# Kernel tuning notes

Measured on AMD Instinct MI355X. Metric: run time of the kernel, lower is better.

The kernel has to match this reference:

```python
import jax, jax.numpy as jnp
import numpy as np

D_MODEL = 1024
N_HEADS = 16
D_K = D_MODEL // N_HEADS
D_FF = 4096
EPS = 1e-5


def setup_inputs() -> dict:
    key = jax.random.key(0)
    ks = jax.random.split(key, 16)
    s = 0.02
    d, f = D_MODEL, D_FF
    return {
        'ebd_x': jax.random.normal(ks[0], (2, 2048, d), jnp.float32),
        'Wq': jax.random.normal(ks[1], (d, d), jnp.float32) * s,
        'bq': jnp.zeros((d,), jnp.float32),
        'Wk': jax.random.normal(ks[2], (d, d), jnp.float32) * s,
        'bk': jnp.zeros((d,), jnp.float32),
        'Wv': jax.random.normal(ks[3], (d, d), jnp.float32) * s,
        'bv': jnp.zeros((d,), jnp.float32),
        'Wo': jax.random.normal(ks[4], (d, d), jnp.float32) * s,
        'bo': jnp.zeros((d,), jnp.float32),
        'W1': jax.random.normal(ks[5], (d, f), jnp.float32) * s,
        'b1': jnp.zeros((f,), jnp.float32),
        'W2': jax.random.normal(ks[6], (f, d), jnp.float32) * s,
        'b2': jnp.zeros((d,), jnp.float32),
        'g1': jnp.ones((d,), jnp.float32),
        'beta1': jnp.zeros((d,), jnp.float32),
        'g2': jnp.ones((d,), jnp.float32),
        'beta2': jnp.zeros((d,), jnp.float32),
    }


def _layernorm(x, g, b):
    mu = jnp.mean(x, axis=-1, keepdims=True)
    var = jnp.mean(jnp.square(x - mu), axis=-1, keepdims=True)
    return (x - mu) * jax.lax.rsqrt(var + EPS) * g + b


def reference(ebd_x, Wq, bq, Wk, bk, Wv, bv, Wo, bo, W1, b1, W2, b2, g1, beta1, g2, beta2):
    b, L, d = ebd_x.shape
    h, dk = N_HEADS, D_K
    # QKV projections, split heads: (b, h, L, dk)
    q = (ebd_x @ Wq + bq).reshape(b, L, h, dk).transpose(0, 2, 1, 3)
    k = (ebd_x @ Wk + bk).reshape(b, L, h, dk).transpose(0, 2, 1, 3)
    v = (ebd_x @ Wv + bv).reshape(b, L, h, dk).transpose(0, 2, 1, 3)
    scores = jnp.einsum('bhLd,bhld->bhLl', q, k) / jnp.sqrt(jnp.float32(dk))
    attn = jax.nn.softmax(scores, axis=-1)
    attn_v = jnp.einsum('bhLl,bhld->bhLd', attn, v)
    # faithful to source: reshape (b,h,L,dk) -> (b,L,d) WITHOUT transposing back
    attn_v = attn_v.reshape(b, L, d)
    attn_v = attn_v @ Wo + bo
    # dropout is identity in eval mode
    x1 = _layernorm(attn_v + ebd_x, g1, beta1)
    ff = jax.nn.gelu(x1 @ W1 + b1, approximate=False) @ W2 + b2
    return _layernorm(ff + x1, g2, beta2)
```

## Files before the change

### kernel.cpp

```cpp
#include <hip/hip_runtime.h>
#include <hip/hip_bf16.h>
#include <math.h>

typedef __bf16 bhalf;
typedef __bf16 bhalf8 __attribute__((ext_vector_type(8)));
typedef float  floatx4 __attribute__((ext_vector_type(4)));
typedef float  floatx8 __attribute__((ext_vector_type(8)));
typedef unsigned short ushort_t;
typedef unsigned short ushort8 __attribute__((ext_vector_type(8)));

#define MFMA16(a, b, c) __builtin_amdgcn_mfma_f32_16x16x32_bf16((a), (b), (c), 0, 0, 0)

__device__ __forceinline__ void gload_lds16(const bhalf* g, bhalf* l)
{
    __builtin_amdgcn_global_load_lds((const __attribute__((address_space(1))) void*)g,
                                     (__attribute__((address_space(3))) void*)l, 16, 0, 0);
}

enum { EPI_PLAIN = 0, EPI_RES = 1, EPI_GELU = 2, EPI_QKV = 3 };

__global__ __launch_bounds__(256) void detect_dtype(const ushort_t* __restrict__ x,
                                                    int* __restrict__ flag)
{
    __shared__ int tot;
    if (threadIdx.x == 0) tot = 0;
    __syncthreads();
    int cnt = 0;
#pragma unroll
    for (int it = 0; it < 8; ++it) {
        const ushort8 u = *(const ushort8*)(x + ((size_t)(it * 256 + threadIdx.x)) * 8);
#pragma unroll
        for (int j = 0; j < 8; j += 2) {
            const int e = (u[j] >> 7) & 0xFF;
            if (e >= 0x90) ++cnt;
        }
    }
    atomicAdd(&tot, cnt);
    __syncthreads();
    if (threadIdx.x == 0) flag[0] = (tot > 64) ? 1 : 0;
}

__global__ __launch_bounds__(256) void norm_x(const void* __restrict__ s,
                                              bhalf* __restrict__ d,
                                              const int* __restrict__ flag)
{
    const int i = (blockIdx.x * 256 + threadIdx.x) * 8;
    if (*flag) {
        const floatx8 v = *(const floatx8*)((const float*)s + i);
        bhalf8 o;
#pragma unroll
        for (int j = 0; j < 8; ++j) o[j] = (bhalf)v[j];
        *(bhalf8*)(d + i) = o;
    } else {
        *(ushort8*)((ushort_t*)d + i) = *(const ushort8*)((const ushort_t*)s + i);
    }
}

struct Cvt { const void* s; bhalf* d; int n; };
struct CvtArr { Cvt t[10]; };

__global__ __launch_bounds__(256) void norm_vec(CvtArr a, const int* __restrict__ flag)
{
    const Cvt c = a.t[blockIdx.y];
    const int i = (blockIdx.x * 256 + threadIdx.x) * 8;
    if (i >= c.n) return;
    if (*flag) {
        const floatx8 v = *(const floatx8*)((const float*)c.s + i);
        bhalf8 o;
#pragma unroll
        for (int j = 0; j < 8; ++j) o[j] = (bhalf)v[j];
        *(bhalf8*)(c.d + i) = o;
    } else {
        *(ushort8*)((ushort_t*)c.d + i) = *(const ushort8*)((const ushort_t*)c.s + i);
    }
}

struct TDesc { const void* src; bhalf* dst; int R, C; };
struct TDescArr { TDesc t[6]; };

__global__ __launch_bounds__(256) void transpose_all(TDescArr a, const int* __restrict__ flag)
{
    __shared__ bhalf sm[32][33];
    const int id = blockIdx.x;
    TDesc d;
    int rem;
    if (id < 4096)      { d = a.t[id >> 10]; rem = id & 1023; }
    else if (id < 8192) { d = a.t[4];        rem = id - 4096; }
    else                { d = a.t[5];        rem = id - 8192; }
    const int txc = d.C >> 5;
    const int bx = (rem % txc) * 32;
    const int by = (rem / txc) * 32;
    const int tx = threadIdx.x & 31;
    const int ty = threadIdx.x >> 5;
    if (*flag) {
        const float* fin = (const float*)d.src;
#pragma unroll
        for (int i = 0; i < 4; ++i)
            sm[ty + i * 8][tx] = (bhalf)fin[(size_t)(by + ty + i * 8) * d.C + bx + tx];
    } else {
        const bhalf* bin = (const bhalf*)d.src;
#pragma unroll
        for (int i = 0; i < 4; ++i)
            sm[ty + i * 8][tx] = bin[(size_t)(by + ty + i * 8) * d.C + bx + tx];
    }
    __syncthreads();
#pragma unroll
    for (int i = 0; i < 4; ++i)
        d.dst[(size_t)(bx + ty + i * 8) * d.R + by + tx] = sm[tx][ty + i * 8];
}

__global__ __launch_bounds__(256) void vt_transpose(const bhalf* __restrict__ Vw,
                                                    bhalf* __restrict__ Vt)
{
    __shared__ bhalf sm[32][33];
    const int bh = blockIdx.z;
    const int b = bh >> 4, h = bh & 15;
    const int tb = blockIdx.y * 32;
    const int db = blockIdx.x * 32;
    const int tx = threadIdx.x & 31;
    const int ty = threadIdx.x >> 5;
#pragma unroll
    for (int i = 0; i < 4; ++i)
        sm[ty + i * 8][tx] = Vw[(size_t)(b * 2048 + tb + ty + i * 8) * 1024 + h * 64 + db + tx];
    __syncthreads();
#pragma unroll
    for (int i = 0; i < 4; ++i)
        Vt[(size_t)(bh * 64 + db + ty + i * 8) * 2048 + tb + tx] = sm[tx][ty + i * 8];
}

template <int EPI, int TN>
__global__ __launch_bounds__(256) void gemm128(
    const bhalf* __restrict__ A, int lda,
    const bhalf* __restrict__ BT, int ldb,
    const bhalf* __restrict__ bias,
    const bhalf* __restrict__ resid,
    bhalf* __restrict__ C, int ldc, int K,
    bhalf* __restrict__ Ck, bhalf* __restrict__ Cv)
{
    __shared__ __align__(16) bhalf As[128 * 64];
    __shared__ __align__(16) bhalf Bs[TN * 64];

    const int tid  = threadIdx.x;
    const int lane = tid & 63;
    const int w    = tid >> 6;
    const int l15  = lane & 15;
    const int q    = lane >> 4;
    constexpr int MT = (TN == 128) ? 4 : 2;
    const int wm   = (TN == 128) ? (w >> 1) * 64 : w * 32;
    const int wn   = (TN == 128) ? (w & 1) * 64 : 0;
    const int n0   = blockIdx.x * TN;
    const int m0   = blockIdx.y * 128;

    const int r8 = lane >> 3;
    const int c8 = lane & 7;
    const int gc = (c8 ^ r8) << 3;

    floatx4 acc[MT][4];
#pragma unroll
    for (int i = 0; i < MT; ++i)
#pragma unroll
        for (int j = 0; j < 4; ++j) acc[i][j] = (floatx4){0.f, 0.f, 0.f, 0.f};

    for (int k0 = 0; k0 < K; k0 += 64) {
        __syncthreads();
#pragma unroll
        for (int i = 0; i < 4; ++i) {
            const int rb = w * 32 + i * 8;
            gload_lds16(A + (size_t)(m0 + rb + r8) * lda + k0 + gc, &As[rb * 64] + lane * 8);
        }
        if constexpr (TN == 128) {
#pragma unroll
            for (int i = 0; i < 4; ++i) {
                const int rb = w * 32 + i * 8;
                gload_lds16(BT + (size_t)(n0 + rb + r8) * ldb + k0 + gc, &Bs[rb * 64] + lane * 8);
            }
        } else {
#pragma unroll
            for (int i = 0; i < 2; ++i) {
                const int rb = w * 16 + i * 8;
                gload_lds16(BT + (size_t)(n0 + rb + r8) * ldb + k0 + gc, &Bs[rb * 64] + lane * 8);
            }
        }
        __syncthreads();
#pragma unroll
        for (int s = 0; s < 2; ++s) {
            const int pc = (((s * 4 + q) ^ (l15 & 7)) << 3);
            bhalf8 af[MT], bf[4];
#pragma unroll
            for (int mt = 0; mt < MT; ++mt)
                af[mt] = *(const bhalf8*)&As[(wm + mt * 16 + l15) * 64 + pc];
#pragma unroll
            for (int nt = 0; nt < 4; ++nt)
                bf[nt] = *(const bhalf8*)&Bs[(wn + nt * 16 + l15) * 64 + pc];
#pragma unroll
            for (int mt = 0; mt < MT; ++mt)
#pragma unroll
                for (int nt = 0; nt < 4; ++nt)
                    acc[mt][nt] = MFMA16(af[mt], bf[nt], acc[mt][nt]);
        }
    }

#pragma unroll
    for (int mt = 0; mt < MT; ++mt)
#pragma unroll
        for (int nt = 0; nt < 4; ++nt) {
            const int col = n0 + wn + nt * 16 + l15;
            const float bv = (float)bias[col];
#pragma unroll
            for (int r = 0; r < 4; ++r) {
                const int row = m0 + wm + mt * 16 + q * 4 + r;
                float v = acc[mt][nt][r] + bv;
                if constexpr (EPI == EPI_PLAIN) {
                    C[(size_t)row * ldc + col] = (bhalf)v;
                } else if constexpr (EPI == EPI_RES) {
                    v += (float)resid[(size_t)row * ldc + col];
                    C[(size_t)row * ldc + col] = (bhalf)v;
                } else if constexpr (EPI == EPI_GELU) {
                    v = 0.5f * v * (1.f + erff(v * 0.70710678118654752f));
                    C[(size_t)row * ldc + col] = (bhalf)v;
                } else {
                    if (col < 1024)       C [(size_t)row * 1024 + col]        = (bhalf)v;
                    else if (col < 2048)  Ck[(size_t)row * 1024 + col - 1024] = (bhalf)v;
                    else                  Cv[(size_t)row * 1024 + col - 2048] = (bhalf)v;
                }
            }
        }
}

__global__ __launch_bounds__(256) void flash_attn(
    const bhalf* __restrict__ Q, const bhalf* __restrict__ Km,
    const bhalf* __restrict__ Vt, bhalf* __restrict__ ctx)
{
    __shared__ __align__(16) bhalf Ks[2][64 * 64];
    __shared__ __align__(16) bhalf Vs[2][64 * 64];
    __shared__ __align__(16) bhalf Ps[64 * 64];

    const int tid  = threadIdx.x;
    const int lane = tid & 63;
    const int wq   = tid >> 6;
    const int l15  = lane & 15;
    const int q    = lane >> 4;
    const int bh   = blockIdx.x & 31;
    const int l0   = (blockIdx.x >> 5) * 64;
    const int b    = bh >> 4, h = bh & 15;
    const float SC = 0.125f * 1.44269504f;

    const bhalf* qp = Q + ((size_t)(b * 2048 + l0 + wq * 16 + l15)) * 1024 + h * 64 + q * 8;
    const bhalf8 aQ0 = *(const bhalf8*)qp;
    const bhalf8 aQ1 = *(const bhalf8*)(qp + 32);

    float ps[4] = {0.f, 0.f, 0.f, 0.f};
    floatx4 o[4];
#pragma unroll
    for (int ot = 0; ot < 4; ++ot) o[ot] = (floatx4){0.f, 0.f, 0.f, 0.f};

    const int r8 = lane >> 3;
    const int c8 = lane & 7;
    const int gc = (c8 ^ r8) << 3;
    const bhalf* kbase = Km + ((size_t)(b * 2048)) * 1024 + h * 64;
    const bhalf* vbase = Vt + ((size_t)(bh * 64)) * 2048;

    auto stage = [&](int buf, int kt) {
#pragma unroll
        for (int i = 0; i < 2; ++i) {
            const int rb = wq * 16 + i * 8;
            gload_lds16(kbase + (size_t)(kt + rb + r8) * 1024 + gc, &Ks[buf][rb * 64] + lane * 8);
            gload_lds16(vbase + (size_t)(rb + r8) * 2048 + kt + gc, &Vs[buf][rb * 64] + lane * 8);
        }
    };

    stage(0, 0);
    int cur = 0;
    for (int kt = 0; kt < 2048; kt += 64) {
        __syncthreads();
        if (kt + 64 < 2048) stage(cur ^ 1, kt + 64);

        floatx4 s[4];
#pragma unroll
        for (int nt = 0; nt < 4; ++nt) {
            s[nt] = (floatx4){0.f, 0.f, 0.f, 0.f};
            bhalf8 bK0 = *(const bhalf8*)&Ks[cur][(nt * 16 + l15) * 64 + ((q ^ (l15 & 7)) << 3)];
            bhalf8 bK1 = *(const bhalf8*)&Ks[cur][(nt * 16 + l15) * 64 + (((4 + q) ^ (l15 & 7)) << 3)];
            s[nt] = MFMA16(aQ0, bK0, s[nt]);
            s[nt] = MFMA16(aQ1, bK1, s[nt]);
        }
#pragma unroll
        for (int nt = 0; nt < 4; ++nt)
#pragma unroll
            for (int r = 0; r < 4; ++r) {
                const float pv = __builtin_amdgcn_exp2f(fmaf(s[nt][r], SC, -8.f));
                ps[r] += pv;
                const int row = wq * 16 + q * 4 + r;
                const int pc = (2 * nt + (l15 >> 3)) ^ ((q * 4 + r) & 7);
                Ps[row * 64 + pc * 8 + (l15 & 7)] = (bhalf)pv;
            }

#pragma unroll
        for (int kc = 0; kc < 2; ++kc) {
            bhalf8 aP = *(const bhalf8*)&Ps[(wq * 16 + l15) * 64 + (((kc * 4 + q) ^ (l15 & 7)) << 3)];
#pragma unroll
            for (int ot = 0; ot < 4; ++ot) {
                bhalf8 bV = *(const bhalf8*)&Vs[cur][(ot * 16 + l15) * 64 + (((kc * 4 + q) ^ (l15 & 7)) << 3)];
                o[ot] = MFMA16(aP, bV, o[ot]);
            }
        }
        cur ^= 1;
    }

    float inv[4];
#pragma unroll
    for (int r = 0; r < 4; ++r) {
#pragma unroll
        for (int off = 1; off < 16; off <<= 1) ps[r] += __shfl_xor(ps[r], off);
        inv[r] = 1.f / ps[r];
    }
#pragma unroll
    for (int ot = 0; ot < 4; ++ot)
#pragma unroll
        for (int r = 0; r < 4; ++r) {
            const int l = l0 + wq * 16 + q * 4 + r;
            const int kk = ot * 16 + l15;
            const int R = h * 128 + (l >> 4);
            const int Cc = (l & 15) * 64 + kk;
            ctx[((size_t)(b * 2048 + R)) * 1024 + Cc] = (bhalf)(o[ot][r] * inv[r]);
        }
}

__global__ __launch_bounds__(256) void ln_kernel(
    const bhalf* __restrict__ X, const bhalf* __restrict__ g,
    const bhalf* __restrict__ be, void* __restrict__ out, const int* __restrict__ flag)
{
    __shared__ float red[4][2];
    const int tid = threadIdx.x;
    const int wid = tid >> 6;
    const int rid = tid >> 7;
    const int lt  = tid & 127;
    const int row = blockIdx.x * 2 + rid;
    const int col = lt * 8;
    const bhalf8 xv = *(const bhalf8*)(X + (size_t)row * 1024 + col);
    float v[8], s1 = 0.f, s2 = 0.f;
#pragma unroll
    for (int i = 0; i < 8; ++i) {
        v[i] = (float)xv[i];
        s1 += v[i];
        s2 += v[i] * v[i];
    }
#pragma unroll
    for (int off = 1; off < 64; off <<= 1) {
        s1 += __shfl_xor(s1, off);
        s2 += __shfl_xor(s2, off);
    }
    if ((tid & 63) == 0) { red[wid][0] = s1; red[wid][1] = s2; }
    __syncthreads();
    const float t1 = red[rid * 2][0] + red[rid * 2 + 1][0];
    const float t2 = red[rid * 2][1] + red[rid * 2 + 1][1];
    const float mu = t1 * (1.f / 1024.f);
    const float rs = rsqrtf(t2 * (1.f / 1024.f) - mu * mu + 1e-5f);
    const bool f32 = flag && (*flag != 0);
    if (f32) {
        floatx8 ov;
#pragma unroll
        for (int i = 0; i < 8; ++i)
            ov[i] = ((v[i] - mu) * rs) * (float)g[col + i] + (float)be[col + i];
        *(floatx8*)((float*)out + (size_t)row * 1024 + col) = ov;
    } else {
        bhalf8 ov;
#pragma unroll
        for (int i = 0; i < 8; ++i)
            ov[i] = (bhalf)(((v[i] - mu) * rs) * (float)g[col + i] + (float)be[col + i]);
        *(bhalf8*)((bhalf*)out + (size_t)row * 1024 + col) = ov;
    }
}

extern "C" void kernel_launch(void* const* d_in, const int* in_sizes, int n_in,
                              void* d_out, int out_size, void* d_ws, size_t ws_size,
                              hipStream_t stream)
{
    (void)in_sizes; (void)n_in; (void)out_size; (void)ws_size;

    char* p = (char*)d_ws;
    const size_t MB = 1024 * 1024;
    int*   flag  = (int*)p;
    bhalf* vecs  = (bhalf*)(p + 128 * 1024);
    bhalf* Qw    = (bhalf*)(p + 1 * MB);
    bhalf* Kw    = (bhalf*)(p + 9 * MB);
    bhalf* Vw    = (bhalf*)(p + 17 * MB);
    bhalf* Vt    = (bhalf*)(p + 25 * MB);
    bhalf* x_n   = (bhalf*)(p + 33 * MB);
    bhalf* WqkvT = (bhalf*)(p + 41 * MB);
    bhalf* WoT   = (bhalf*)(p + 47 * MB);
    bhalf* W1T   = (bhalf*)(p + 49 * MB);
    bhalf* W2T   = (bhalf*)(p + 57 * MB);
    bhalf* ctx   = Vw;
    bhalf* ff1   = (bhalf*)(p + 17 * MB);
    bhalf* ln1   = Qw;
    bhalf* x1    = Kw;
    bhalf* ff2   = Qw;

    bhalf* bqkv  = vecs;
    bhalf* bo_n  = vecs + 1 * 4096;
    bhalf* b1_n  = vecs + 2 * 4096;
    bhalf* b2_n  = vecs + 3 * 4096;
    bhalf* g1_n  = vecs + 4 * 4096;
    bhalf* be1_n = vecs + 5 * 4096;
    bhalf* g2_n  = vecs + 6 * 4096;
    bhalf* be2_n = vecs + 7 * 4096;

    const dim3 blk(256);

    detect_dtype<<<1, blk, 0, stream>>>((const ushort_t*)d_in[0], flag);

    norm_x<<<2048, blk, 0, stream>>>(d_in[0], x_n, flag);
    CvtArr arr;
    arr.t[0] = {d_in[2],  bqkv,        1024};
    arr.t[1] = {d_in[4],  bqkv + 1024, 1024};
    arr.t[2] = {d_in[6],  bqkv + 2048, 1024};
    arr.t[3] = {d_in[8],  bo_n,        1024};
    arr.t[4] = {d_in[10], b1_n,        4096};
    arr.t[5] = {d_in[12], b2_n,        1024};
    arr.t[6] = {d_in[13], g1_n,        1024};
    arr.t[7] = {d_in[14], be1_n,       1024};
    arr.t[8] = {d_in[15], g2_n,        1024};
    arr.t[9] = {d_in[16], be2_n,       1024};
    norm_vec<<<dim3(2, 10), blk, 0, stream>>>(arr, flag);

    TDescArr td;
    td.t[0] = {d_in[1],  WqkvT,               1024, 1024};
    td.t[1] = {d_in[3],  WqkvT + 1024 * 1024, 1024, 1024};
    td.t[2] = {d_in[5],  WqkvT + 2048 * 1024, 1024, 1024};
    td.t[3] = {d_in[7],  WoT,                 1024, 1024};
    td.t[4] = {d_in[9],  W1T,                 1024, 4096};
    td.t[5] = {d_in[11], W2T,                 4096, 1024};
    transpose_all<<<12288, blk, 0, stream>>>(td, flag);

    gemm128<EPI_QKV, 128><<<dim3(24, 32), blk, 0, stream>>>(
        x_n, 1024, WqkvT, 1024, bqkv, nullptr, Qw, 1024, 1024, Kw, Vw);

    vt_transpose<<<dim3(2, 64, 32), blk, 0, stream>>>(Vw, Vt);

    flash_attn<<<1024, blk, 0, stream>>>(Qw, Kw, Vt, ctx);

    gemm128<EPI_RES, 64><<<dim3(16, 32), blk, 0, stream>>>(
        ctx, 1024, WoT, 1024, bo_n, x_n, ln1, 1024, 1024, nullptr, nullptr);
    ln_kernel<<<2048, blk, 0, stream>>>(ln1, g1_n, be1_n, x1, nullptr);

    gemm128<EPI_GELU, 128><<<dim3(32, 32), blk, 0, stream>>>(
        x1, 1024, W1T, 1024, b1_n, nullptr, ff1, 4096, 1024, nullptr, nullptr);
    gemm128<EPI_RES, 64><<<dim3(16, 32), blk, 0, stream>>>(
        ff1, 4096, W2T, 4096, b2_n, x1, ff2, 1024, 4096, nullptr, nullptr);
    ln_kernel<<<2048, blk, 0, stream>>>(ff2, g2_n, be2_n, d_out, flag);
}
```

Measured before the change: 391.1 us.

## Pre-pack weights into MFMA fragment layout and stream B directly from global

Weight transposes now write directly into a packed layout in which each 16-row by 32-k block is one contiguous 512-element fragment. The GEMMs load B operands straight from global memory into registers, which removes the B shared-memory staging. A is now double-buffered in LDS and the next tile is prefetched during compute. Each wave covers 32 rows by the full N tile, and exact erff in the GELU epilogue is replaced by a polynomial erf approximation. The price is more global traffic per wave for B, since there is no cross-wave sharing through LDS, plus slightly lower GELU accuracy.

```diff
diff --git a/kernel.cpp b/kernel.cpp
--- a/kernel.cpp
+++ b/kernel.cpp
@@ -17,6 +17,16 @@
                                      (__attribute__((address_space(3))) void*)l, 16, 0, 0);
 }
 
+__device__ __forceinline__ float erf_poly(float x)
+{
+    const float ax = fabsf(x);
+    const float t = 1.f / fmaf(0.3275911f, ax, 1.f);
+    const float y = t * fmaf(t, fmaf(t, fmaf(t, fmaf(t, 1.061405429f, -1.453152027f),
+                                             1.421413741f), -0.284496736f), 0.254829592f);
+    const float e = __builtin_amdgcn_exp2f(-ax * ax * 1.44269504f);
+    return copysignf(fmaf(-y, e, 1.f), x);
+}
+
 enum { EPI_PLAIN = 0, EPI_RES = 1, EPI_GELU = 2, EPI_QKV = 3 };
 
 __global__ __launch_bounds__(256) void detect_dtype(const ushort_t* __restrict__ x,
@@ -78,7 +88,7 @@
 struct TDesc { const void* src; bhalf* dst; int R, C; };
 struct TDescArr { TDesc t[6]; };
 
-__global__ __launch_bounds__(256) void transpose_all(TDescArr a, const int* __restrict__ flag)
+__global__ __launch_bounds__(256) void pack_all(TDescArr a, const int* __restrict__ flag)
 {
     __shared__ bhalf sm[32][33];
     const int id = blockIdx.x;
@@ -104,9 +114,13 @@
             sm[ty + i * 8][tx] = bin[(size_t)(by + ty + i * 8) * d.C + bx + tx];
     }
     __syncthreads();
-#pragma unroll
-    for (int i = 0; i < 4; ++i)
-        d.dst[(size_t)(bx + ty + i * 8) * d.R + by + tx] = sm[tx][ty + i * 8];
+    const int kc32 = d.R >> 5;
+#pragma unroll
+    for (int i = 0; i < 4; ++i) {
+        const int n = bx + ty + i * 8;
+        const size_t base = ((size_t)(n >> 4) * kc32 + (by >> 5)) * 512;
+        d.dst[base + (((tx >> 3) * 16 + (n & 15)) << 3) + (tx & 7)] = sm[tx][ty + i * 8];
+    }
 }
 
 __global__ __launch_bounds__(256) void vt_transpose(const bhalf* __restrict__ Vw,
@@ -128,83 +142,79 @@
         Vt[(size_t)(bh * 64 + db + ty + i * 8) * 2048 + tb + tx] = sm[tx][ty + i * 8];
 }
 
-template <int EPI, int TN>
-__global__ __launch_bounds__(256) void gemm128(
+template <int EPI, int NT>
+__global__ __launch_bounds__(256) void gemm_pk(
     const bhalf* __restrict__ A, int lda,
-    const bhalf* __restrict__ BT, int ldb,
+    const bhalf* __restrict__ BP,
     const bhalf* __restrict__ bias,
     const bhalf* __restrict__ resid,
     bhalf* __restrict__ C, int ldc, int K,
     bhalf* __restrict__ Ck, bhalf* __restrict__ Cv)
 {
-    __shared__ __align__(16) bhalf As[128 * 64];
-    __shared__ __align__(16) bhalf Bs[TN * 64];
+    __shared__ __align__(16) bhalf As[2][128 * 64];
 
     const int tid  = threadIdx.x;
     const int lane = tid & 63;
     const int w    = tid >> 6;
     const int l15  = lane & 15;
     const int q    = lane >> 4;
-    constexpr int MT = (TN == 128) ? 4 : 2;
-    const int wm   = (TN == 128) ? (w >> 1) * 64 : w * 32;
-    const int wn   = (TN == 128) ? (w & 1) * 64 : 0;
-    const int n0   = blockIdx.x * TN;
+    const int wm   = w * 32;
+    const int n0   = blockIdx.x * (NT * 16);
     const int m0   = blockIdx.y * 128;
 
     const int r8 = lane >> 3;
     const int c8 = lane & 7;
     const int gc = (c8 ^ r8) << 3;
-
-    floatx4 acc[MT][4];
-#pragma unroll
-    for (int i = 0; i < MT; ++i)
-#pragma unroll
-        for (int j = 0; j < 4; ++j) acc[i][j] = (floatx4){0.f, 0.f, 0.f, 0.f};
-
+    const int kc32 = K >> 5;
+    const bhalf* bpb = BP + (size_t)(n0 >> 4) * kc32 * 512 + lane * 8;
+
+    floatx4 acc[2][NT];
+#pragma unroll
+    for (int i = 0; i < 2; ++i)
+#pragma unroll
+        for (int j = 0; j < NT; ++j) acc[i][j] = (floatx4){0.f, 0.f, 0.f, 0.f};
+
+    auto stageA = [&](int buf, int k0) {
+#pragma unroll
+        for (int i = 0; i < 4; ++i) {
+            const int rb = w * 32 + i * 8;
+            gload_lds16(A + (size_t)(m0 + rb + r8) * lda + k0 + gc,
+                        &As[buf][rb * 64] + lane * 8);
+        }
+    };
+
+    stageA(0, 0);
+    int cur = 0;
     for (int k0 = 0; k0 < K; k0 += 64) {
         __syncthreads();
-#pragma unroll
-        for (int i = 0; i < 4; ++i) {
-            const int rb = w * 32 + i * 8;
-            gload_lds16(A + (size_t)(m0 + rb + r8) * lda + k0 + gc, &As[rb * 64] + lane * 8);
-        }
-        if constexpr (TN == 128) {
-#pragma unroll
-            for (int i = 0; i < 4; ++i) {
-                const int rb = w * 32 + i * 8;
-                gload_lds16(BT + (size_t)(n0 + rb + r8) * ldb + k0 + gc, &Bs[rb * 64] + lane * 8);
-            }
-        } else {
-#pragma unroll
-            for (int i = 0; i < 2; ++i) {
-                const int rb = w * 16 + i * 8;
-                gload_lds16(BT + (size_t)(n0 + rb + r8) * ldb + k0 + gc, &Bs[rb * 64] + lane * 8);
-            }
-        }
-        __syncthreads();
+        bhalf8 bf[2][NT];
+#pragma unroll
+        for (int s = 0; s < 2; ++s)
+#pragma unroll
+            for (int nt = 0; nt < NT; ++nt)
+                bf[s][nt] = *(const bhalf8*)(bpb + (size_t)(nt * kc32 + (k0 >> 5) + s) * 512);
+        if (k0 + 64 < K) stageA(cur ^ 1, k0 + 64);
 #pragma unroll
         for (int s = 0; s < 2; ++s) {
             const int pc = (((s * 4 + q) ^ (l15 & 7)) << 3);
-            bhalf8 af[MT], bf[4];
-#pragma unroll
-            for (int mt = 0; mt < MT; ++mt)
-                af[mt] = *(const bhalf8*)&As[(wm + mt * 16 + l15) * 64 + pc];
-#pragma unroll
-            for (int nt = 0; nt < 4; ++nt)
-                bf[nt] = *(const bhalf8*)&Bs[(wn + nt * 16 + l15) * 64 + pc];
-#pragma unroll
-            for (int mt = 0; mt < MT; ++mt)
-#pragma unroll
-                for (int nt = 0; nt < 4; ++nt)
-                    acc[mt][nt] = MFMA16(af[mt], bf[nt], acc[mt][nt]);
-        }
-    }
-
-#pragma unroll
-    for (int mt = 0; mt < MT; ++mt)
-#pragma unroll
-        for (int nt = 0; nt < 4; ++nt) {
-            const int col = n0 + wn + nt * 16 + l15;
+            bhalf8 af[2];
+#pragma unroll
+            for (int mt = 0; mt < 2; ++mt)
+                af[mt] = *(const bhalf8*)&As[cur][(wm + mt * 16 + l15) * 64 + pc];
+#pragma unroll
+            for (int mt = 0; mt < 2; ++mt)
+#pragma unroll
+                for (int nt = 0; nt < NT; ++nt)
+                    acc[mt][nt] = MFMA16(af[mt], bf[s][nt], acc[mt][nt]);
+        }
+        cur ^= 1;
+    }
+
+#pragma unroll
+    for (int mt = 0; mt < 2; ++mt)
+#pragma unroll
+        for (int nt = 0; nt < NT; ++nt) {
+            const int col = n0 + nt * 16 + l15;
             const float bv = (float)bias[col];
 #pragma unroll
             for (int r = 0; r < 4; ++r) {
@@ -216,7 +226,7 @@
                     v += (float)resid[(size_t)row * ldc + col];
                     C[(size_t)row * ldc + col] = (bhalf)v;
                 } else if constexpr (EPI == EPI_GELU) {
-                    v = 0.5f * v * (1.f + erff(v * 0.70710678118654752f));
+                    v = 0.5f * v * (1.f + erf_poly(v * 0.70710678118654752f));
                     C[(size_t)row * ldc + col] = (bhalf)v;
                 } else {
                     if (col < 1024)       C [(size_t)row * 1024 + col]        = (bhalf)v;
@@ -387,10 +397,10 @@
     bhalf* Vw    = (bhalf*)(p + 17 * MB);
     bhalf* Vt    = (bhalf*)(p + 25 * MB);
     bhalf* x_n   = (bhalf*)(p + 33 * MB);
-    bhalf* WqkvT = (bhalf*)(p + 41 * MB);
-    bhalf* WoT   = (bhalf*)(p + 47 * MB);
-    bhalf* W1T   = (bhalf*)(p + 49 * MB);
-    bhalf* W2T   = (bhalf*)(p + 57 * MB);
+    bhalf* WqkvP = (bhalf*)(p + 41 * MB);
+    bhalf* WoP   = (bhalf*)(p + 47 * MB);
+    bhalf* W1P   = (bhalf*)(p + 49 * MB);
+    bhalf* W2P   = (bhalf*)(p + 57 * MB);
     bhalf* ctx   = Vw;
     bhalf* ff1   = (bhalf*)(p + 17 * MB);
     bhalf* ln1   = Qw;
@@ -425,28 +435,28 @@
     norm_vec<<<dim3(2, 10), blk, 0, stream>>>(arr, flag);
 
     TDescArr td;
-    td.t[0] = {d_in[1],  WqkvT,               1024, 1024};
-    td.t[1] = {d_in[3],  WqkvT + 1024 * 1024, 1024, 1024};
-    td.t[2] = {d_in[5],  WqkvT + 2048 * 1024, 1024, 1024};
-    td.t[3] = {d_in[7],  WoT,                 1024, 1024};
-    td.t[4] = {d_in[9],  W1T,                 1024, 4096};
-    td.t[5] = {d_in[11], W2T,                 4096, 1024};
-    transpose_all<<<12288, blk, 0, stream>>>(td, flag);
-
-    gemm128<EPI_QKV, 128><<<dim3(24, 32), blk, 0, stream>>>(
-        x_n, 1024, WqkvT, 1024, bqkv, nullptr, Qw, 1024, 1024, Kw, Vw);
+    td.t[0] = {d_in[1],  WqkvP,               1024, 1024};
+    td.t[1] = {d_in[3],  WqkvP + 1024 * 1024, 1024, 1024};
+    td.t[2] = {d_in[5],  WqkvP + 2048 * 1024, 1024, 1024};
+    td.t[3] = {d_in[7],  WoP,                 1024, 1024};
+    td.t[4] = {d_in[9],  W1P,                 1024, 4096};
+    td.t[5] = {d_in[11], W2P,                 4096, 1024};
+    pack_all<<<12288, blk, 0, stream>>>(td, flag);
+
+    gemm_pk<EPI_QKV, 8><<<dim3(24, 32), blk, 0, stream>>>(
+        x_n, 1024, WqkvP, bqkv, nullptr, Qw, 1024, 1024, Kw, Vw);
 
     vt_transpose<<<dim3(2, 64, 32), blk, 0, stream>>>(Vw, Vt);
 
     flash_attn<<<1024, blk, 0, stream>>>(Qw, Kw, Vt, ctx);
 
-    gemm128<EPI_RES, 64><<<dim3(16, 32), blk, 0, stream>>>(
-        ctx, 1024, WoT, 1024, bo_n, x_n, ln1, 1024, 1024, nullptr, nullptr);
+    gemm_pk<EPI_RES, 4><<<dim3(16, 32), blk, 0, stream>>>(
+        ctx, 1024, WoP, bo_n, x_n, ln1, 1024, 1024, nullptr, nullptr);
     ln_kernel<<<2048, blk, 0, stream>>>(ln1, g1_n, be1_n, x1, nullptr);
 
-    gemm128<EPI_GELU, 128><<<dim3(32, 32), blk, 0, stream>>>(
-        x1, 1024, W1T, 1024, b1_n, nullptr, ff1, 4096, 1024, nullptr, nullptr);
-    gemm128<EPI_RES, 64><<<dim3(16, 32), blk, 0, stream>>>(
-        ff1, 4096, W2T, 4096, b2_n, x1, ff2, 1024, 4096, nullptr, nullptr);
+    gemm_pk<EPI_GELU, 8><<<dim3(32, 32), blk, 0, stream>>>(
+        x1, 1024, W1P, b1_n, nullptr, ff1, 4096, 1024, nullptr, nullptr);
+    gemm_pk<EPI_RES, 4><<<dim3(16, 32), blk, 0, stream>>>(
+        ff1, 4096, W2P, b2_n, x1, ff2, 1024, 4096, nullptr, nullptr);
     ln_kernel<<<2048, blk, 0, stream>>>(ff2, g2_n, be2_n, d_out, flag);
 }
```

Result: slower. 432.6 us (+10.6%).
